# Kernel tuning notes

Measured on AMD Instinct MI355X. Metric: run time of the kernel, lower is better.

## Reference

```python
import jax, jax.numpy as jnp
import numpy as np

N0, N1, N2 = 32768, 8192, 2048
DEG = 8
E0, E1, E2 = N0 * DEG, N1 * DEG, N2 * DEG
C = 32
OUT = 40
EPS = 1e-9


def setup_inputs() -> dict:
    key = jax.random.key(0)
    ks = jax.random.split(key, 32)
    w = lambda k, s, sc=0.1: jax.random.normal(k, s, jnp.float32) * sc
    d = {}
    d['pos0'] = jax.random.normal(ks[0], (N0, 3), jnp.float32)
    d['v0'] = jax.random.normal(ks[1], (N0, 1, 3), jnp.float32)
    # attention layer weights: 10 layers total (2 per block x 5 blocks)
    d['Wq_first'] = w(ks[2], (1, C)); d['Wk_first'] = w(ks[3], (1, C))
    d['Wv_first'] = w(ks[4], (1, C)); d['Wskip_first'] = w(ks[5], (1, C))
    d['Wq_mid'] = w(ks[6], (8, C, C)); d['Wk_mid'] = w(ks[7], (8, C, C))
    d['Wv_mid'] = w(ks[8], (8, C, C)); d['Wskip_mid'] = w(ks[9], (8, C, C))
    d['Wq_last'] = w(ks[10], (C, 1)); d['Wk_last'] = w(ks[11], (C, 1))
    d['Wv_last'] = w(ks[12], (C, 1)); d['Wskip_last'] = w(ks[13], (C, 1))
    d['wr1'] = w(ks[14], (10, 1, 16)); d['wr2'] = w(ks[15], (10, 16, 1))
    d['scale_mid'] = jnp.ones((9, C), jnp.float32)
    d['bias_mid'] = jnp.zeros((9, C), jnp.float32)
    d['scale_last'] = jnp.ones((1,), jnp.float32)
    d['bias_last'] = jnp.zeros((1,), jnp.float32)
    d['Wmlp'] = w(ks[16], (3, OUT))
    d['src0'] = jax.random.randint(ks[17], (E0,), 0, N0)
    d['dst0'] = jax.random.randint(ks[18], (E0,), 0, N0)
    d['src1'] = jax.random.randint(ks[19], (E1,), 0, N1)
    d['dst1'] = jax.random.randint(ks[20], (E1,), 0, N1)
    d['src2'] = jax.random.randint(ks[21], (E2,), 0, N2)
    d['dst2'] = jax.random.randint(ks[22], (E2,), 0, N2)
    d['fp_idx1'] = jax.random.permutation(ks[23], N0)[:N1]
    d['fp_idx2'] = jax.random.permutation(ks[24], N1)[:N2]
    d['cluster1'] = jax.random.randint(ks[25], (N0,), 0, N1)
    d['cluster2'] = jax.random.randint(ks[26], (N1,), 0, N2)
    return d


def _attn(x, src, dst, rel, r, Wq, Wk, Wv, Ws, w1, w2, n):
    # x: [n, Cin, 3] type-1 fiber; equivariant linear maps mix channels only
    q = jnp.einsum('ncv,co->nov', x, Wq)
    k = jnp.einsum('ncv,co->nov', x, Wk)
    v = jnp.einsum('ncv,co->nov', x, Wv)
    logits = jnp.einsum('eov,eov->e', q[dst], k[src]) / np.float32(np.sqrt(3.0 * Wq.shape[1]))
    logits = logits + (jax.nn.relu(r @ w1) @ w2)[:, 0]  # radial (invariant) edge bias
    m = jax.ops.segment_max(logits, dst, num_segments=n)
    ex = jnp.exp(logits - m[dst])
    z = jax.ops.segment_sum(ex, dst, num_segments=n)
    alpha = ex / (z[dst] + EPS)
    msg = (v[src] + rel[:, None, :]) * alpha[:, None, None]  # x_ij='add'
    agg = jax.ops.segment_sum(msg, dst, num_segments=n)
    return agg + jnp.einsum('ncv,co->nov', x, Ws)  # learnable skip


def _norm_bias(x, scale, bias):
    # GNormBias: nonlinearity on invariant norm, preserve direction
    nrm = jnp.sqrt(jnp.sum(x * x, axis=-1, keepdims=True) + 1e-12)
    return jax.nn.relu(scale[None, :, None] * nrm + bias[None, :, None]) * (x / nrm)


def _segmean(x, seg, n):
    s = jax.ops.segment_sum(x, seg, num_segments=n)
    c = jax.ops.segment_sum(jnp.ones((seg.shape[0], 1, 1), x.dtype), seg, num_segments=n)
    return s / (c + EPS)


def reference(pos0, v0, Wq_first, Wk_first, Wv_first, Wskip_first, Wq_mid, Wk_mid, Wv_mid, Wskip_mid, Wq_last, Wk_last, Wv_last, Wskip_last, wr1, wr2, scale_mid, bias_mid, scale_last, bias_last, Wmlp, src0, dst0, src1, dst1, src2, dst2, fp_idx1, fp_idx2, cluster1, cluster2):
    def edge_geo(pos, src, dst):
        rel = pos[dst] - pos[src]
        r = jnp.sqrt(jnp.sum(rel * rel, -1, keepdims=True) + 1e-12)
        return rel, r

    rel0, r0 = edge_geo(pos0, src0, dst0)
    pos1 = pos0[fp_idx1]
    rel1, r1 = edge_geo(pos1, src1, dst1)
    pos2 = pos1[fp_idx2]
    rel2, r2 = edge_geo(pos2, src2, dst2)

    def layer(i, x, Wq, Wk, Wv, Ws, sc, bi, src, dst, rel, r, n):
        return _norm_bias(_attn(x, src, dst, rel, r, Wq, Wk, Wv, Ws, wr1[i], wr2[i], n), sc, bi)

    # down block 0 (level 0)
    x = layer(0, v0, Wq_first, Wk_first, Wv_first, Wskip_first, scale_mid[0], bias_mid[0], src0, dst0, rel0, r0, N0)
    x0 = layer(1, x, Wq_mid[0], Wk_mid[0], Wv_mid[0], Wskip_mid[0], scale_mid[1], bias_mid[1], src0, dst0, rel0, r0, N0)
    # FPS pool -> level 1, down block 1
    x = _segmean(x0, cluster1, N1)
    x = layer(2, x, Wq_mid[1], Wk_mid[1], Wv_mid[1], Wskip_mid[1], scale_mid[2], bias_mid[2], src1, dst1, rel1, r1, N1)
    x1 = layer(3, x, Wq_mid[2], Wk_mid[2], Wv_mid[2], Wskip_mid[2], scale_mid[3], bias_mid[3], src1, dst1, rel1, r1, N1)
    # FPS pool -> level 2, bottleneck
    x = _segmean(x1, cluster2, N2)
    x = layer(4, x, Wq_mid[3], Wk_mid[3], Wv_mid[3], Wskip_mid[3], scale_mid[4], bias_mid[4], src2, dst2, rel2, r2, N2)
    x = layer(5, x, Wq_mid[4], Wk_mid[4], Wv_mid[4], Wskip_mid[4], scale_mid[5], bias_mid[5], src2, dst2, rel2, r2, N2)
    # upsample to level 1 via fp_idx scatter + residual skip, up block 0
    x = jnp.zeros((N1, C, 3), x.dtype).at[fp_idx2].set(x) + x1
    x = layer(6, x, Wq_mid[5], Wk_mid[5], Wv_mid[5], Wskip_mid[5], scale_mid[6], bias_mid[6], src1, dst1, rel1, r1, N1)
    x = layer(7, x, Wq_mid[6], Wk_mid[6], Wv_mid[6], Wskip_mid[6], scale_mid[7], bias_mid[7], src1, dst1, rel1, r1, N1)
    # upsample to level 0 + residual skip, up block 1 (out fiber {1:1})
    x = jnp.zeros((N0, C, 3), x.dtype).at[fp_idx1].set(x) + x0
    x = layer(8, x, Wq_mid[7], Wk_mid[7], Wv_mid[7], Wskip_mid[7], scale_mid[8], bias_mid[8], src0, dst0, rel0, r0, N0)
    x = layer(9, x, Wq_last, Wk_last, Wv_last, Wskip_last, scale_last, bias_last, src0, dst0, rel0, r0, N0)
    # MLP head: [N0,1,3] -> (B=1, N0, 3) -> Linear(3, OUT, no bias) + ReLU
    y = jax.nn.relu(jnp.einsum('bnf,fo->bno', x.reshape(1, N0, 3), Wmlp))
    return y
```

## Files before the change

### kernel.cpp

```cpp
#include <hip/hip_runtime.h>
#include <math.h>

#define N0 32768
#define N1 8192
#define N2 2048
#define E0 262144
#define E1 65536
#define E2 16384
#define NTOT (N0+N1+N2)
#define ETOT (E0+E1+E2)
#define NBLK (NTOT/256)
#define EPS 1e-9f

static inline int cdiv(int a, int b){ return (a + b - 1) / b; }

__device__ inline unsigned bfpack(float a, float b){
  unsigned ua = __float_as_uint(a), ub = __float_as_uint(b);
  ua = (ua + 0x7fffu + ((ua >> 16) & 1u)) >> 16;
  ub = (ub + 0x7fffu + ((ub >> 16) & 1u)) & 0xffff0000u;
  return ua | ub;
}
__device__ inline float bf_lo(unsigned d){ return __uint_as_float(d << 16); }
__device__ inline float bf_hi(unsigned d){ return __uint_as_float(d & 0xffff0000u); }

__device__ inline float grp32_sum(float x){
  x += __int_as_float(__builtin_amdgcn_update_dpp(0, __float_as_int(x), 0x121, 0xf, 0xf, true));
  x += __int_as_float(__builtin_amdgcn_update_dpp(0, __float_as_int(x), 0x122, 0xf, 0xf, true));
  x += __int_as_float(__builtin_amdgcn_update_dpp(0, __float_as_int(x), 0x124, 0xf, 0xf, true));
  x += __int_as_float(__builtin_amdgcn_update_dpp(0, __float_as_int(x), 0x128, 0xf, 0xf, true));
  x += __int_as_float(__builtin_amdgcn_ds_swizzle(__float_as_int(x), 0x401F));
  return x;
}

__global__ void k_setup(const int* __restrict__ d0, const int* __restrict__ d1,
                        const int* __restrict__ d2,
                        const int* __restrict__ fp1, const int* __restrict__ fp2,
                        int* cnt, int* __restrict__ inv0, int* __restrict__ inv1){
  int e = blockIdx.x*256 + threadIdx.x;
  if (e < E0)            atomicAdd(&cnt[d0[e]], 1);
  else if (e < E0+E1)    atomicAdd(&cnt[N0 + d1[e-E0]], 1);
  else if (e < ETOT)     atomicAdd(&cnt[N0+N1 + d2[e-E0-E1]], 1);
  if (e < N1) inv0[fp1[e]] = e;
  if (e < N2) inv1[fp2[e]] = e;
}
__global__ __launch_bounds__(256) void k_scan1(const int* __restrict__ cnt,
                                               int* __restrict__ excl,
                                               int* __restrict__ bsum){
  __shared__ int lds[256];
  int tid = threadIdx.x;
  int i = blockIdx.x*256 + tid;
  int v = cnt[i];
  lds[tid] = v;
  __syncthreads();
  for (int off = 1; off < 256; off <<= 1){
    int t = (tid >= off) ? lds[tid - off] : 0;
    __syncthreads();
    lds[tid] += t;
    __syncthreads();
  }
  excl[i] = lds[tid] - v;
  if (tid == 255) bsum[blockIdx.x] = lds[255];
}
__global__ __launch_bounds__(256) void k_scan23(const int* __restrict__ excl,
                                                const int* __restrict__ bsum,
                                                int* __restrict__ row,
                                                int* __restrict__ cur){
  __shared__ int lds[256];
  int tid = threadIdx.x;
  int v = (tid < (int)blockIdx.x && tid < NBLK) ? bsum[tid] : 0;
  lds[tid] = v;
  __syncthreads();
  for (int off = 1; off < 256; off <<= 1){
    int t = (tid >= off) ? lds[tid - off] : 0;
    __syncthreads();
    lds[tid] += t;
    __syncthreads();
  }
  int offset = lds[255];
  int i = blockIdx.x*256 + tid;
  int r = excl[i] + offset;
  row[i] = r; cur[i] = r;
  if (i == 0) row[NTOT] = ETOT;
}
__global__ void k_scatter_geoA(const int* __restrict__ s0, const int* __restrict__ d0,
                               const int* __restrict__ s1, const int* __restrict__ d1,
                               const int* __restrict__ s2, const int* __restrict__ d2,
                               const float* __restrict__ pos0,
                               const int* __restrict__ fp1, const int* __restrict__ fp2,
                               const float* __restrict__ w1, const float* __restrict__ w2,
                               int* cur, int* __restrict__ srcs, float4* __restrict__ meta,
                               float* __restrict__ rb9){
  int e = blockIdx.x*256 + threadIdx.x;
  if (e >= ETOT) return;
  int s, d, noff, sp, dp;
  if (e < E0){
    s = s0[e]; d = d0[e]; noff = 0;
    sp = s; dp = d;
  } else if (e < E0+E1){
    s = s1[e-E0]; d = d1[e-E0]; noff = N0;
    sp = fp1[s]; dp = fp1[d];
  } else {
    s = s2[e-E0-E1]; d = d2[e-E0-E1]; noff = N0+N1;
    sp = fp1[fp2[s]]; dp = fp1[fp2[d]];
  }
  float dx = pos0[dp*3+0]-pos0[sp*3+0];
  float dy = pos0[dp*3+1]-pos0[sp*3+1];
  float dz = pos0[dp*3+2]-pos0[sp*3+2];
  float r = sqrtf(dx*dx+dy*dy+dz*dz+1e-12f);
  int p = atomicAdd(&cur[noff + d], 1);
  srcs[p] = s;
  meta[p] = make_float4(r, dx, dy, dz);
  if (p < E0){
    float a = 0.f;
    #pragma unroll
    for (int j = 0; j < 16; ++j) a += fmaxf(r*w1[j], 0.f)*w2[j];
    rb9[p] = a;
  }
}

__global__ __launch_bounds__(256) void k_transformF(
    const float* __restrict__ x, const float* __restrict__ cntv,
    const float* __restrict__ up, const int* __restrict__ inv,
    const float* __restrict__ Wq, const float* __restrict__ Wk,
    const float* __restrict__ Wv, const float* __restrict__ Ws,
    float* __restrict__ q, unsigned* __restrict__ kv, float* __restrict__ s,
    int n, int Cin, int mode){
  __shared__ float wI[4096];
  __shared__ float xr4[8][128];
  __shared__ float kvst[8][192];
  int tid = threadIdx.x;
  int nw = Cin * 32;
  for (int i = tid; i < nw; i += 256){
    wI[i*4+0] = Wq[i]; wI[i*4+1] = Wk[i]; wI[i*4+2] = Wv[i]; wI[i*4+3] = Ws[i];
  }
  int g = tid >> 5, lane = tid & 31;
  int node = blockIdx.x*8 + g;
  int xl = Cin * 3;
  if (node < n){
    if (mode == 1){
      float ic = 1.f / (cntv[node] + EPS);
      for (int c = lane; c < Cin; c += 32){
        int b = node*xl + c*3;
        xr4[g][c*4+0] = x[b+0]*ic; xr4[g][c*4+1] = x[b+1]*ic; xr4[g][c*4+2] = x[b+2]*ic;
      }
    } else if (mode == 2){
      int a = inv[node];
      for (int c = lane; c < Cin; c += 32){
        int b = node*xl + c*3;
        float v0_ = x[b], v1_ = x[b+1], v2_ = x[b+2];
        if (a >= 0){
          size_t ub = (size_t)a*xl + c*3;
          v0_ += up[ub]; v1_ += up[ub+1]; v2_ += up[ub+2];
        }
        xr4[g][c*4+0] = v0_; xr4[g][c*4+1] = v1_; xr4[g][c*4+2] = v2_;
      }
    } else {
      for (int c = lane; c < Cin; c += 32){
        int b = node*xl + c*3;
        xr4[g][c*4+0] = x[b]; xr4[g][c*4+1] = x[b+1]; xr4[g][c*4+2] = x[b+2];
      }
    }
  }
  __syncthreads();
  if (node < n){
    float aq0=0.f,aq1=0.f,aq2=0.f, ak0=0.f,ak1=0.f,ak2=0.f;
    float aw0=0.f,aw1=0.f,aw2=0.f, as0=0.f,as1=0.f,as2=0.f;
    for (int c = 0; c < Cin; ++c){
      float4 xv = *(const float4*)&xr4[g][c*4];
      float4 wv = *(const float4*)&wI[(c*32+lane)*4];
      aq0 += xv.x*wv.x; aq1 += xv.y*wv.x; aq2 += xv.z*wv.x;
      ak0 += xv.x*wv.y; ak1 += xv.y*wv.y; ak2 += xv.z*wv.y;
      aw0 += xv.x*wv.z; aw1 += xv.y*wv.z; aw2 += xv.z*wv.z;
      as0 += xv.x*wv.w; as1 += xv.y*wv.w; as2 += xv.z*wv.w;
    }
    int o = node*96 + lane*3;
    q[o]=aq0; q[o+1]=aq1; q[o+2]=aq2;
    s[o]=as0; s[o+1]=as1; s[o+2]=as2;
    kvst[g][lane*3+0]=ak0; kvst[g][lane*3+1]=ak1; kvst[g][lane*3+2]=ak2;
    kvst[g][96+lane*3+0]=aw0; kvst[g][96+lane*3+1]=aw1; kvst[g][96+lane*3+2]=aw2;
    float2 p0 = *(const float2*)&kvst[g][2*lane];
    float2 p1 = *(const float2*)&kvst[g][64+2*lane];
    float2 p2 = *(const float2*)&kvst[g][128+2*lane];
    *(uint2*)(kv + (size_t)node*96 + 2*lane) = make_uint2(bfpack(p0.x,p0.y), bfpack(p1.x,p1.y));
    kv[(size_t)node*96 + 64 + lane] = bfpack(p2.x, p2.y);
  }
}

#define ATTN_CORE(QB,KVB,SB) \
  float rw1 = (lane < 16) ? wr1[lane] : 0.f; \
  float rw2 = (lane < 16) ? wr2[lane] : 0.f; \
  float ql0=0.f, ql1=0.f, ql2=0.f, ql3=0.f; \
  float z=0.f, av0=0.f, av1=0.f, av2=0.f, av3=0.f, R0=0.f, R1=0.f, R2=0.f; \
  int beg=0, end=0; \
  if (act){ \
    int nb = node*96; \
    float2 qa = *(const float2*)(QB + nb + 2*lane); \
    ql0 = qa.x*invsc; ql1 = qa.y*invsc; \
    if (lane < 16){ \
      float2 qc = *(const float2*)(QB + nb + 64 + 2*lane); \
      ql2 = qc.x*invsc; ql3 = qc.y*invsc; \
    } \
    beg = row[node]; end = row[node+1]; \
  } \
  for (int cb = beg; cb < end; cb += 32){ \
    int csz = end - cb; if (csz > 32) csz = 32; \
    int sn_l = 0; float4 mt = make_float4(0.f,0.f,0.f,0.f); \
    if (lane < csz){ \
      int idx = cb + lane; \
      sn_l = srcs[idx]; \
      mt = meta[idx]; \
    } \
    for (int j = 0; j < csz; j += 4){ \
      int gs = csz - j; if (gs > 4) gs = 4; \
      int sid[4]; float rrB[4]; \
      _Pragma("unroll") \
      for (int t = 0; t < 4; ++t){ \
        int sl = (j + t) & 31; \
        sid[t] = __shfl(sn_l, sl, 32); \
        rrB[t] = __shfl(mt.x, sl, 32); \
      } \
      unsigned d0[4], d1[4], d2[4]; \
      _Pragma("unroll") \
      for (int t = 0; t < 4; ++t){ \
        const unsigned* kp = KVB + (size_t)sid[t]*96; \
        bool ok = t < gs; \
        uint2 ab = ok ? *(const uint2*)(kp + 2*lane) : make_uint2(0u,0u); \
        d0[t] = ab.x; d1[t] = ab.y; \
        d2[t] = ok ? kp[64 + lane] : 0u; \
      } \
      _Pragma("unroll") \
      for (int t = 0; t < 4; ++t){ \
        float pt = bf_lo(d0[t])*ql0 + bf_hi(d0[t])*ql1; \
        if (lane < 16) pt += bf_lo(d1[t])*ql2 + bf_hi(d1[t])*ql3; \
        pt += fmaxf(rrB[t]*rw1, 0.f) * rw2; \
        pt = grp32_sum(pt); \
        float w = (t < gs) ? __expf(fminf(pt, 80.f)) : 0.f; \
        z += w; \
        av0 += w*bf_lo(d2[t]); av1 += w*bf_hi(d2[t]); \
        if (lane >= 16){ av2 += w*bf_lo(d1[t]); av3 += w*bf_hi(d1[t]); } \
        if (lane == j + t){ R0 += w*mt.y; R1 += w*mt.z; R2 += w*mt.w; } \
      } \
    } \
  } \
  R0 = grp32_sum(R0); \
  R1 = grp32_sum(R1); \
  R2 = grp32_sum(R2); \
  if (act){ \
    vsum[g][2*lane+32] = av0; \
    vsum[g][2*lane+33] = av1; \
    if (lane >= 16){ vsum[g][2*lane-32] = av2; vsum[g][2*lane-31] = av3; } \
  } \
  float y0=0.f, y1=0.f, y2=0.f; \
  if (act){ \
    float invz = 1.f / (z + EPS); \
    int base = node*96 + 3*lane; \
    y0 = (vsum[g][3*lane+0] + R0)*invz + SB[base]; \
    y1 = (vsum[g][3*lane+1] + R1)*invz + SB[base+1]; \
    y2 = (vsum[g][3*lane+2] + R2)*invz + SB[base+2]; \
    float nrm = sqrtf(y0*y0 + y1*y1 + y2*y2 + 1e-12f); \
    float f = fmaxf(scaleA[lane]*nrm + biasA[lane], 0.f) / nrm; \
    y0 *= f; y1 *= f; y2 *= f; \
  }

__global__ __launch_bounds__(256) void k_attn32(
    const float* __restrict__ qb, const unsigned* __restrict__ kvb,
    const float* __restrict__ sb,
    const int* __restrict__ row, const int* __restrict__ srcs,
    const float4* __restrict__ meta,
    const float* __restrict__ wr1, const float* __restrict__ wr2,
    const float* __restrict__ scaleA, const float* __restrict__ biasA,
    float* __restrict__ outb,
    float* psum, float* pcnt_, const int* __restrict__ cl,
    int n, float invsc){
  __shared__ float vsum[8][96];
  int tid = threadIdx.x, g = tid >> 5, lane = tid & 31;
  int node = blockIdx.x*8 + g;
  bool act = node < n;
  ATTN_CORE(qb, kvb, sb)
  if (act){
    int base = node*96 + 3*lane;
    outb[base]   = y0;
    outb[base+1] = y1;
    outb[base+2] = y2;
    if (cl){
      int c = cl[node];
      atomicAdd(&psum[c*96 + 3*lane],   y0);
      atomicAdd(&psum[c*96 + 3*lane+1], y1);
      atomicAdd(&psum[c*96 + 3*lane+2], y2);
      if (lane == 0) atomicAdd(&pcnt_[c], 1.f);
    }
  }
}

__global__ __launch_bounds__(256) void k_attn32_t32(
    float* __restrict__ qb, const unsigned* __restrict__ kvin,
    float* __restrict__ sb,
    const int* __restrict__ row, const int* __restrict__ srcs,
    const float4* __restrict__ meta,
    const float* __restrict__ wr1, const float* __restrict__ wr2,
    const float* __restrict__ scaleA, const float* __restrict__ biasA,
    const float* __restrict__ Wq2, const float* __restrict__ Wk2,
    const float* __restrict__ Wv2, const float* __restrict__ Ws2,
    unsigned* __restrict__ kvout, int n, float invsc){
  __shared__ float vsum[8][96];
  __shared__ float wI[4096];
  __shared__ float kvst[8][192];
  int tid = threadIdx.x, g = tid >> 5, lane = tid & 31;
  for (int i = tid; i < 1024; i += 256){
    wI[i*4+0] = Wq2[i]; wI[i*4+1] = Wk2[i]; wI[i*4+2] = Wv2[i]; wI[i*4+3] = Ws2[i];
  }
  int node = blockIdx.x*8 + g;
  bool act = node < n;
  ATTN_CORE(qb, kvin, sb)
  __syncthreads();
  if (act){
    vsum[g][3*lane+0] = y0;
    vsum[g][3*lane+1] = y1;
    vsum[g][3*lane+2] = y2;
    float aq0=0.f,aq1=0.f,aq2=0.f, ak0=0.f,ak1=0.f,ak2=0.f;
    float aw0=0.f,aw1=0.f,aw2=0.f, as0=0.f,as1=0.f,as2=0.f;
    for (int c = 0; c < 32; ++c){
      float x0 = vsum[g][c*3+0], x1 = vsum[g][c*3+1], x2 = vsum[g][c*3+2];
      float4 wv = *(const float4*)&wI[(c*32+lane)*4];
      aq0 += x0*wv.x;  aq1 += x1*wv.x;  aq2 += x2*wv.x;
      ak0 += x0*wv.y;  ak1 += x1*wv.y;  ak2 += x2*wv.y;
      aw0 += x0*wv.z;  aw1 += x1*wv.z;  aw2 += x2*wv.z;
      as0 += x0*wv.w;  as1 += x1*wv.w;  as2 += x2*wv.w;
    }
    int ob = node*96 + 3*lane;
    qb[ob]=aq0; qb[ob+1]=aq1; qb[ob+2]=aq2;
    sb[ob]=as0; sb[ob+1]=as1; sb[ob+2]=as2;
    kvst[g][lane*3+0]=ak0; kvst[g][lane*3+1]=ak1; kvst[g][lane*3+2]=ak2;
    kvst[g][96+lane*3+0]=aw0; kvst[g][96+lane*3+1]=aw1; kvst[g][96+lane*3+2]=aw2;
    float2 p0 = *(const float2*)&kvst[g][2*lane];
    float2 p1 = *(const float2*)&kvst[g][64+2*lane];
    float2 p2 = *(const float2*)&kvst[g][128+2*lane];
    *(uint2*)(kvout + (size_t)node*96 + 2*lane) = make_uint2(bfpack(p0.x,p0.y), bfpack(p1.x,p1.y));
    kvout[(size_t)node*96 + 64 + lane] = bfpack(p2.x, p2.y);
  }
}

__global__ __launch_bounds__(256) void k_attn32_t1(
    const float* __restrict__ qb, const unsigned* __restrict__ kvin,
    const float* __restrict__ sb,
    const int* __restrict__ row, const int* __restrict__ srcs,
    const float4* __restrict__ meta,
    const float* __restrict__ wr1, const float* __restrict__ wr2,
    const float* __restrict__ scaleA, const float* __restrict__ biasA,
    const float* __restrict__ Wq2, const float* __restrict__ Wk2,
    const float* __restrict__ Wv2, const float* __restrict__ Ws2,
    float* __restrict__ q1, float* __restrict__ kv1,
    float* __restrict__ s1,
    int n, float invsc){
  __shared__ float vsum[8][96];
  int tid = threadIdx.x, g = tid >> 5, lane = tid & 31;
  int node = blockIdx.x*8 + g;
  bool act = node < n;
  ATTN_CORE(qb, kvin, sb)
  if (act){
    vsum[g][3*lane+0] = y0;
    vsum[g][3*lane+1] = y1;
    vsum[g][3*lane+2] = y2;
  }
  if (act && lane < 12){
    int m = lane / 3, v = lane - m*3;
    const float* W = (m==0) ? Wq2 : (m==1) ? Wk2 : (m==2) ? Wv2 : Ws2;
    float a = 0.f;
    for (int c = 0; c < 32; ++c) a += vsum[g][c*3+v] * W[c];
    if (m==0)      q1[node*3 + v] = a;
    else if (m==1) kv1[(size_t)node*8 + v] = a;
    else if (m==2) kv1[(size_t)node*8 + 3 + v] = a;
    else           s1[node*3 + v] = a;
  }
}

__global__ __launch_bounds__(256) void k_attn1_head(
    const float* __restrict__ qb, const float* __restrict__ kv1,
    const float* __restrict__ sb, const float* __restrict__ rb9,
    const int* __restrict__ row, const int* __restrict__ srcs,
    const float4* __restrict__ meta,
    const float* __restrict__ scaleA, const float* __restrict__ biasA,
    const float* __restrict__ Wmlp,
    float* __restrict__ out, int n, float invsc){
  __shared__ float w[120];
  int tid = threadIdx.x;
  if (tid < 120) w[tid] = Wmlp[tid];
  __syncthreads();
  int i = blockIdx.x*32 + (tid >> 3);
  int lane8 = tid & 7;
  if (i >= n) return;
  float q0 = qb[i*3]*invsc, q1 = qb[i*3+1]*invsc, q2 = qb[i*3+2]*invsc;
  float z = 0.f, a0 = 0.f, a1 = 0.f, a2 = 0.f;
  int beg = row[i], end = row[i+1];
  for (int e = beg + lane8; e < end; e += 8){
    int s = srcs[e];
    float4 m = meta[e];
    float4 A = *(const float4*)(kv1 + (size_t)s*8);
    float2 B = *(const float2*)(kv1 + (size_t)s*8 + 4);
    float pt = q0*A.x + q1*A.y + q2*A.z + rb9[e];
    float wgt = __expf(fminf(pt, 80.f));
    z += wgt;
    a0 += wgt*(A.w + m.y); a1 += wgt*(B.x + m.z); a2 += wgt*(B.y + m.w);
  }
  #pragma unroll
  for (int xm = 1; xm <= 4; xm <<= 1){
    z  += __shfl_xor(z,  xm, 8);
    a0 += __shfl_xor(a0, xm, 8);
    a1 += __shfl_xor(a1, xm, 8);
    a2 += __shfl_xor(a2, xm, 8);
  }
  float invz = 1.f / (z + EPS);
  float y0 = a0*invz + sb[i*3];
  float y1 = a1*invz + sb[i*3+1];
  float y2 = a2*invz + sb[i*3+2];
  float nrm = sqrtf(y0*y0 + y1*y1 + y2*y2 + 1e-12f);
  float f = fmaxf(scaleA[0]*nrm + biasA[0], 0.f) / nrm;
  y0 *= f; y1 *= f; y2 *= f;
  #pragma unroll
  for (int c = 0; c < 5; ++c){
    int o2 = lane8*5 + c;
    out[(size_t)i*40 + o2] = fmaxf(y0*w[o2] + y1*w[40+o2] + y2*w[80+o2], 0.f);
  }
}

extern "C" void kernel_launch(void* const* d_in, const int* in_sizes, int n_in,
                              void* d_out, int out_size, void* d_ws, size_t ws_size,
                              hipStream_t stream){
  const float* pos0      = (const float*)d_in[0];
  const float* v0        = (const float*)d_in[1];
  const float* Wq_first  = (const float*)d_in[2];
  const float* Wk_first  = (const float*)d_in[3];
  const float* Wv_first  = (const float*)d_in[4];
  const float* Ws_first  = (const float*)d_in[5];
  const float* Wq_mid    = (const float*)d_in[6];
  const float* Wk_mid    = (const float*)d_in[7];
  const float* Wv_mid    = (const float*)d_in[8];
  const float* Ws_mid    = (const float*)d_in[9];
  const float* Wq_last   = (const float*)d_in[10];
  const float* Wk_last   = (const float*)d_in[11];
  const float* Wv_last   = (const float*)d_in[12];
  const float* Ws_last   = (const float*)d_in[13];
  const float* wr1       = (const float*)d_in[14];
  const float* wr2       = (const float*)d_in[15];
  const float* scale_mid = (const float*)d_in[16];
  const float* bias_mid  = (const float*)d_in[17];
  const float* scale_last= (const float*)d_in[18];
  const float* bias_last = (const float*)d_in[19];
  const float* Wmlp      = (const float*)d_in[20];
  const int* src0 = (const int*)d_in[21];
  const int* dst0 = (const int*)d_in[22];
  const int* src1 = (const int*)d_in[23];
  const int* dst1 = (const int*)d_in[24];
  const int* src2 = (const int*)d_in[25];
  const int* dst2 = (const int*)d_in[26];
  const int* fp1  = (const int*)d_in[27];
  const int* fp2  = (const int*)d_in[28];
  const int* cl1  = (const int*)d_in[29];
  const int* cl2  = (const int*)d_in[30];

  float* ws = (float*)d_ws;
  size_t o = 0;
  float* xA   = ws + o; o += (size_t)N0*96;
  float* x0s  = ws + o; o += (size_t)N0*96;
  float* x1s  = ws + o; o += (size_t)N1*96;
  float* qb   = ws + o; o += (size_t)N0*96;
  float* sb   = ws + o; o += (size_t)N0*96;
  unsigned* kvb  = (unsigned*)(ws + o); o += (size_t)N0*96;
  unsigned* kvb2 = (unsigned*)(ws + o); o += (size_t)N0*96;
  float4* metaA = (float4*)(ws + o); o += (size_t)ETOT*4;
  float* q1v  = ws + o; o += (size_t)N0*3;
  float* s1v  = ws + o; o += (size_t)N0*3;
  float* kv1  = ws + o; o += (size_t)N0*8;
  float* rb9  = ws + o; o += (size_t)E0;
  float* zz   = ws + o;
  float* xP1  = ws + o; o += (size_t)N1*96;
  float* xP2  = ws + o; o += (size_t)N2*96;
  float* pcnt1 = ws + o; o += N1;
  float* pcnt2 = ws + o; o += N2;
  int* cntA = (int*)(ws + o); o += NTOT;
  size_t zz_bytes = ((size_t)N1*96 + N2*96 + N1 + N2 + NTOT) * sizeof(float);
  int* ib = (int*)(ws + o);
  size_t io = 0;
  int* rowA  = ib + io; io += NTOT+1;
  int* curA  = ib + io; io += NTOT;
  int* exclA = ib + io; io += NTOT;
  int* bsumA = ib + io; io += 256;
  int* srcsA = ib + io; io += ETOT;
  int* inv0  = ib + io; io += N0;
  int* inv1  = ib + io; io += N1;
  size_t ff_bytes = ((size_t)N0 + N1) * sizeof(int);

  hipMemsetAsync(zz, 0, zz_bytes, stream);
  hipMemsetAsync(inv0, 0xFF, ff_bytes, stream);

  k_setup<<<cdiv(ETOT,256),256,0,stream>>>(dst0, dst1, dst2, fp1, fp2, cntA, inv0, inv1);
  k_scan1<<<NBLK,256,0,stream>>>(cntA, exclA, bsumA);
  k_scan23<<<NBLK,256,0,stream>>>(exclA, bsumA, rowA, curA);
  k_scatter_geoA<<<cdiv(ETOT,256),256,0,stream>>>(src0, dst0, src1, dst1, src2, dst2,
                                                  pos0, fp1, fp2,
                                                  wr1 + 9*16, wr2 + 9*16,
                                                  curA, srcsA, metaA, rb9);

  const float invsc = 1.f / sqrtf(96.f);
  const int C = 32;

  auto pair32 = [&](const float* xin, const float* cntv, const float* up, const int* inv,
                    int mode, int n, int nodeBase, int Cin,
                    const float* WqE, const float* WkE, const float* WvE, const float* WsE,
                    const float* WqO, const float* WkO, const float* WvO, const float* WsO,
                    int lE, float* xout,
                    float* psum, float* pcnt_, const int* cl){
    k_transformF<<<cdiv(n,8),256,0,stream>>>(xin, cntv, up, inv, WqE, WkE, WvE, WsE,
                                             qb, kvb, sb, n, Cin, mode);
    k_attn32_t32<<<cdiv(n,8),256,0,stream>>>(qb, kvb, sb, rowA + nodeBase, srcsA, metaA,
                                             wr1 + lE*16, wr2 + lE*16,
                                             scale_mid + lE*C, bias_mid + lE*C,
                                             WqO, WkO, WvO, WsO, kvb2, n, invsc);
    k_attn32<<<cdiv(n,8),256,0,stream>>>(qb, kvb2, sb, rowA + nodeBase, srcsA, metaA,
                                         wr1 + (lE+1)*16, wr2 + (lE+1)*16,
                                         scale_mid + (lE+1)*C, bias_mid + (lE+1)*C,
                                         xout, psum, pcnt_, cl, n, invsc);
  };

  pair32(v0, nullptr, nullptr, nullptr, 0, N0, 0, 1,
         Wq_first, Wk_first, Wv_first, Ws_first,
         Wq_mid+0*1024, Wk_mid+0*1024, Wv_mid+0*1024, Ws_mid+0*1024,
         0, x0s, xP1, pcnt1, cl1);
  pair32(xP1, pcnt1, nullptr, nullptr, 1, N1, N0, C,
         Wq_mid+1*1024, Wk_mid+1*1024, Wv_mid+1*1024, Ws_mid+1*1024,
         Wq_mid+2*1024, Wk_mid+2*1024, Wv_mid+2*1024, Ws_mid+2*1024,
         2, x1s, xP2, pcnt2, cl2);
  pair32(xP2, pcnt2, nullptr, nullptr, 1, N2, N0+N1, C,
         Wq_mid+3*1024, Wk_mid+3*1024, Wv_mid+3*1024, Ws_mid+3*1024,
         Wq_mid+4*1024, Wk_mid+4*1024, Wv_mid+4*1024, Ws_mid+4*1024,
         4, xA, nullptr, nullptr, nullptr);
  pair32(x1s, nullptr, xA, inv1, 2, N1, N0, C,
         Wq_mid+5*1024, Wk_mid+5*1024, Wv_mid+5*1024, Ws_mid+5*1024,
         Wq_mid+6*1024, Wk_mid+6*1024, Wv_mid+6*1024, Ws_mid+6*1024,
         6, xA, nullptr, nullptr, nullptr);
  k_transformF<<<cdiv(N0,8),256,0,stream>>>(x0s, nullptr, xA, inv0,
                                            Wq_mid+7*1024, Wk_mid+7*1024,
                                            Wv_mid+7*1024, Ws_mid+7*1024,
                                            qb, kvb, sb, N0, C, 2);
  k_attn32_t1<<<cdiv(N0,8),256,0,stream>>>(qb, kvb, sb, rowA, srcsA, metaA,
                                           wr1 + 8*16, wr2 + 8*16,
                                           scale_mid + 8*C, bias_mid + 8*C,
                                           Wq_last, Wk_last, Wv_last, Ws_last,
                                           q1v, kv1, s1v, N0, invsc);
  {
    float invsc1 = 1.f / sqrtf(3.f);
    k_attn1_head<<<cdiv(N0,32),256,0,stream>>>(q1v, kv1, s1v, rb9, rowA, srcsA, metaA,
                                               scale_last, bias_last,
                                               Wmlp, (float*)d_out, N0, invsc1);
  }
}
```

Baseline: 403.0 us.

## Replace atomic cluster pooling with CSR gather-based segment mean

Cluster pooling used to be done with float atomicAdd scatter into pooled buffers from the attention epilogue. It now builds CSR lists of cluster members during setup, reusing the existing count/scan/scatter pipeline with extra segments. The next level's transform kernel then gathers and averages member features directly. This removes the contended float atomics and the memset of the pooled buffers, at the cost of irregular gathers in the transform and a larger scan.

```diff
diff --git a/kernel.cpp b/kernel.cpp
--- a/kernel.cpp
+++ b/kernel.cpp
@@ -9,7 +9,9 @@
 #define E2 16384
 #define NTOT (N0+N1+N2)
 #define ETOT (E0+E1+E2)
-#define NBLK (NTOT/256)
+#define DTOT (NTOT+N1+N2)
+#define NBLK2 (DTOT/256)
+#define SLOTS (ETOT+N0+N1)
 #define EPS 1e-9f
 
 static inline int cdiv(int a, int b){ return (a + b - 1) / b; }
@@ -35,12 +37,17 @@
 __global__ void k_setup(const int* __restrict__ d0, const int* __restrict__ d1,
                         const int* __restrict__ d2,
                         const int* __restrict__ fp1, const int* __restrict__ fp2,
+                        const int* __restrict__ cl1, const int* __restrict__ cl2,
                         int* cnt, int* __restrict__ inv0, int* __restrict__ inv1){
   int e = blockIdx.x*256 + threadIdx.x;
   if (e < E0)            atomicAdd(&cnt[d0[e]], 1);
   else if (e < E0+E1)    atomicAdd(&cnt[N0 + d1[e-E0]], 1);
   else if (e < ETOT)     atomicAdd(&cnt[N0+N1 + d2[e-E0-E1]], 1);
-  if (e < N1) inv0[fp1[e]] = e;
+  if (e < N0) atomicAdd(&cnt[NTOT + cl1[e]], 1);
+  if (e < N1){
+    atomicAdd(&cnt[NTOT + N1 + cl2[e]], 1);
+    inv0[fp1[e]] = e;
+  }
   if (e < N2) inv1[fp2[e]] = e;
 }
 __global__ __launch_bounds__(256) void k_scan1(const int* __restrict__ cnt,
@@ -67,7 +74,7 @@
                                                 int* __restrict__ cur){
   __shared__ int lds[256];
   int tid = threadIdx.x;
-  int v = (tid < (int)blockIdx.x && tid < NBLK) ? bsum[tid] : 0;
+  int v = (tid < (int)blockIdx.x && tid < NBLK2) ? bsum[tid] : 0;
   lds[tid] = v;
   __syncthreads();
   for (int off = 1; off < 256; off <<= 1){
@@ -80,18 +87,27 @@
   int i = blockIdx.x*256 + tid;
   int r = excl[i] + offset;
   row[i] = r; cur[i] = r;
-  if (i == 0) row[NTOT] = ETOT;
+  if (i == 0) row[DTOT] = SLOTS;
 }
 __global__ void k_scatter_geoA(const int* __restrict__ s0, const int* __restrict__ d0,
                                const int* __restrict__ s1, const int* __restrict__ d1,
                                const int* __restrict__ s2, const int* __restrict__ d2,
                                const float* __restrict__ pos0,
                                const int* __restrict__ fp1, const int* __restrict__ fp2,
+                               const int* __restrict__ cl1, const int* __restrict__ cl2,
                                const float* __restrict__ w1, const float* __restrict__ w2,
-                               int* cur, int* __restrict__ srcs, float4* __restrict__ meta,
+                               int* cur, int* __restrict__ slots, float4* __restrict__ meta,
                                float* __restrict__ rb9){
   int e = blockIdx.x*256 + threadIdx.x;
   if (e >= ETOT) return;
+  if (e < N0){
+    int p = atomicAdd(&cur[NTOT + cl1[e]], 1);
+    slots[p] = e;
+  }
+  if (e < N1){
+    int p = atomicAdd(&cur[NTOT + N1 + cl2[e]], 1);
+    slots[p] = e;
+  }
   int s, d, noff, sp, dp;
   if (e < E0){
     s = s0[e]; d = d0[e]; noff = 0;
@@ -108,7 +124,7 @@
   float dz = pos0[dp*3+2]-pos0[sp*3+2];
   float r = sqrtf(dx*dx+dy*dy+dz*dz+1e-12f);
   int p = atomicAdd(&cur[noff + d], 1);
-  srcs[p] = s;
+  slots[p] = s;
   meta[p] = make_float4(r, dx, dy, dz);
   if (p < E0){
     float a = 0.f;
@@ -119,7 +135,7 @@
 }
 
 __global__ __launch_bounds__(256) void k_transformF(
-    const float* __restrict__ x, const float* __restrict__ cntv,
+    const float* __restrict__ x, const int* __restrict__ rowC, const int* __restrict__ slots,
     const float* __restrict__ up, const int* __restrict__ inv,
     const float* __restrict__ Wq, const float* __restrict__ Wk,
     const float* __restrict__ Wv, const float* __restrict__ Ws,
@@ -138,10 +154,16 @@
   int xl = Cin * 3;
   if (node < n){
     if (mode == 1){
-      float ic = 1.f / (cntv[node] + EPS);
+      int mb = rowC[node], me = rowC[node+1];
+      float ic = 1.f / ((float)(me - mb) + EPS);
       for (int c = lane; c < Cin; c += 32){
-        int b = node*xl + c*3;
-        xr4[g][c*4+0] = x[b+0]*ic; xr4[g][c*4+1] = x[b+1]*ic; xr4[g][c*4+2] = x[b+2]*ic;
+        float s0 = 0.f, s1 = 0.f, s2 = 0.f;
+        for (int m = mb; m < me; ++m){
+          int id = slots[m];
+          int b = id*xl + c*3;
+          s0 += x[b]; s1 += x[b+1]; s2 += x[b+2];
+        }
+        xr4[g][c*4+0] = s0*ic; xr4[g][c*4+1] = s1*ic; xr4[g][c*4+2] = s2*ic;
       }
     } else if (mode == 2){
       int a = inv[node];
@@ -270,7 +292,6 @@
     const float* __restrict__ wr1, const float* __restrict__ wr2,
     const float* __restrict__ scaleA, const float* __restrict__ biasA,
     float* __restrict__ outb,
-    float* psum, float* pcnt_, const int* __restrict__ cl,
     int n, float invsc){
   __shared__ float vsum[8][96];
   int tid = threadIdx.x, g = tid >> 5, lane = tid & 31;
@@ -282,13 +303,6 @@
     outb[base]   = y0;
     outb[base+1] = y1;
     outb[base+2] = y2;
-    if (cl){
-      int c = cl[node];
-      atomicAdd(&psum[c*96 + 3*lane],   y0);
-      atomicAdd(&psum[c*96 + 3*lane+1], y1);
-      atomicAdd(&psum[c*96 + 3*lane+2], y2);
-      if (lane == 0) atomicAdd(&pcnt_[c], 1.f);
-    }
   }
 }
 
@@ -472,84 +486,79 @@
   float* s1v  = ws + o; o += (size_t)N0*3;
   float* kv1  = ws + o; o += (size_t)N0*8;
   float* rb9  = ws + o; o += (size_t)E0;
-  float* zz   = ws + o;
-  float* xP1  = ws + o; o += (size_t)N1*96;
-  float* xP2  = ws + o; o += (size_t)N2*96;
-  float* pcnt1 = ws + o; o += N1;
-  float* pcnt2 = ws + o; o += N2;
-  int* cntA = (int*)(ws + o); o += NTOT;
-  size_t zz_bytes = ((size_t)N1*96 + N2*96 + N1 + N2 + NTOT) * sizeof(float);
+  int* cntA = (int*)(ws + o); o += DTOT;
   int* ib = (int*)(ws + o);
   size_t io = 0;
-  int* rowA  = ib + io; io += NTOT+1;
-  int* curA  = ib + io; io += NTOT;
-  int* exclA = ib + io; io += NTOT;
+  int* rowA  = ib + io; io += DTOT+1;
+  int* curA  = ib + io; io += DTOT;
+  int* exclA = ib + io; io += DTOT;
   int* bsumA = ib + io; io += 256;
-  int* srcsA = ib + io; io += ETOT;
+  int* slotsA = ib + io; io += SLOTS;
   int* inv0  = ib + io; io += N0;
   int* inv1  = ib + io; io += N1;
   size_t ff_bytes = ((size_t)N0 + N1) * sizeof(int);
 
-  hipMemsetAsync(zz, 0, zz_bytes, stream);
+  hipMemsetAsync(cntA, 0, (size_t)DTOT*sizeof(int), stream);
   hipMemsetAsync(inv0, 0xFF, ff_bytes, stream);
 
-  k_setup<<<cdiv(ETOT,256),256,0,stream>>>(dst0, dst1, dst2, fp1, fp2, cntA, inv0, inv1);
-  k_scan1<<<NBLK,256,0,stream>>>(cntA, exclA, bsumA);
-  k_scan23<<<NBLK,256,0,stream>>>(exclA, bsumA, rowA, curA);
+  k_setup<<<cdiv(ETOT,256),256,0,stream>>>(dst0, dst1, dst2, fp1, fp2, cl1, cl2,
+                                           cntA, inv0, inv1);
+  k_scan1<<<NBLK2,256,0,stream>>>(cntA, exclA, bsumA);
+  k_scan23<<<NBLK2,256,0,stream>>>(exclA, bsumA, rowA, curA);
   k_scatter_geoA<<<cdiv(ETOT,256),256,0,stream>>>(src0, dst0, src1, dst1, src2, dst2,
-                                                  pos0, fp1, fp2,
+                                                  pos0, fp1, fp2, cl1, cl2,
                                                   wr1 + 9*16, wr2 + 9*16,
-                                                  curA, srcsA, metaA, rb9);
+                                                  curA, slotsA, metaA, rb9);
 
   const float invsc = 1.f / sqrtf(96.f);
   const int C = 32;
 
-  auto pair32 = [&](const float* xin, const float* cntv, const float* up, const int* inv,
+  auto pair32 = [&](const float* xin, const int* rowC, const float* up, const int* inv,
                     int mode, int n, int nodeBase, int Cin,
                     const float* WqE, const float* WkE, const float* WvE, const float* WsE,
                     const float* WqO, const float* WkO, const float* WvO, const float* WsO,
-                    int lE, float* xout,
-                    float* psum, float* pcnt_, const int* cl){
-    k_transformF<<<cdiv(n,8),256,0,stream>>>(xin, cntv, up, inv, WqE, WkE, WvE, WsE,
+                    int lE, float* xout){
+    k_transformF<<<cdiv(n,8),256,0,stream>>>(xin, rowC, slotsA, up, inv,
+                                             WqE, WkE, WvE, WsE,
                                              qb, kvb, sb, n, Cin, mode);
-    k_attn32_t32<<<cdiv(n,8),256,0,stream>>>(qb, kvb, sb, rowA + nodeBase, srcsA, metaA,
+    k_attn32_t32<<<cdiv(n,8),256,0,stream>>>(qb, kvb, sb, rowA + nodeBase, slotsA, metaA,
                                              wr1 + lE*16, wr2 + lE*16,
                                              scale_mid + lE*C, bias_mid + lE*C,
                                              WqO, WkO, WvO, WsO, kvb2, n, invsc);
-    k_attn32<<<cdiv(n,8),256,0,stream>>>(qb, kvb2, sb, rowA + nodeBase, srcsA, metaA,
+    k_attn32<<<cdiv(n,8),256,0,stream>>>(qb, kvb2, sb, rowA + nodeBase, slotsA, metaA,
                                          wr1 + (lE+1)*16, wr2 + (lE+1)*16,
                                          scale_mid + (lE+1)*C, bias_mid + (lE+1)*C,
-                                         xout, psum, pcnt_, cl, n, invsc);
+                                         xout, n, invsc);
   };
 
   pair32(v0, nullptr, nullptr, nullptr, 0, N0, 0, 1,
          Wq_first, Wk_first, Wv_first, Ws_first,
          Wq_mid+0*1024, Wk_mid+0*1024, Wv_mid+0*1024, Ws_mid+0*1024,
-         0, x0s, xP1, pcnt1, cl1);
-  pair32(xP1, pcnt1, nullptr, nullptr, 1, N1, N0, C,
+         0, x0s);
+  pair32(x0s, rowA + NTOT, nullptr, nullptr, 1, N1, N0, C,
          Wq_mid+1*1024, Wk_mid+1*1024, Wv_mid+1*1024, Ws_mid+1*1024,
          Wq_mid+2*1024, Wk_mid+2*1024, Wv_mid+2*1024, Ws_mid+2*1024,
-         2, x1s, xP2, pcnt2, cl2);
-  pair32(xP2, pcnt2, nullptr, nullptr, 1, N2, N0+N1, C,
+         2, x1s);
+  pair32(x1s, rowA + NTOT + N1, nullptr, nullptr, 1, N2, N0+N1, C,
          Wq_mid+3*1024, Wk_mid+3*1024, Wv_mid+3*1024, Ws_mid+3*1024,
          Wq_mid+4*1024, Wk_mid+4*1024, Wv_mid+4*1024, Ws_mid+4*1024,
-         4, xA, nullptr, nullptr, nullptr);
+         4, xA);
   pair32(x1s, nullptr, xA, inv1, 2, N1, N0, C,
          Wq_mid+5*1024, Wk_mid+5*1024, Wv_mid+5*1024, Ws_mid+5*1024,
          Wq_mid+6*1024, Wk_mid+6*1024, Wv_mid+6*1024, Ws_mid+6*1024,
-         6, xA, nullptr, nullptr, nullptr);
-  k_transformF<<<cdiv(N0,8),256,0,stream>>>(x0s, nullptr, xA, inv0,
+         6, xA);
+  k_transformF<<<cdiv(N0,8),256,0,stream>>>(x0s, nullptr, slotsA, xA, inv0,
                                             Wq_mid+7*1024, Wk_mid+7*1024,
                                             Wv_mid+7*1024, Ws_mid+7*1024,
                                             qb, kvb, sb, N0, C, 2);
-  k_attn32_t1<<<cdiv(N0,8),256,0,stream>>>(qb, kvb, sb, rowA, srcsA, metaA,
+  k_attn32_t1<<<cdiv(N0,8),256,0,stream>>>(qb, kvb, sb, rowA, slotsA, metaA,
                                            wr1 + 8*16, wr2 + 8*16,
                                            scale_mid + 8*C, bias_mid + 8*C,
                                            Wq_last, Wk_last, Wv_last, Ws_last,
                                            q1v, kv1, s1v, N0, invsc);
   {
     float invsc1 = 1.f / sqrtf(3.f);
-    k_attn1_head<<<cdiv(N0,32),256,0,stream>>>(q1v, kv1, s1v, rb9, rowA, srcsA, metaA,
+    k_attn1_head<<<cdiv(N0,32),256,0,stream>>>(q1v, kv1, s1v, rb9, rowA, slotsA, metaA,
                                                scale_last, bias_last,
                                                Wmlp, (float*)d_out, N0, invsc1);
   }
```

Measured after the change: 386.3 us, median of 2. -4.1%, faster.
